# Performance work log

Hardware: AMD Instinct MI355X
Metric: run time of the kernel (lower is better)

Reference implementation:

```python
import jax, jax.numpy as jnp
import numpy as np

N_NODES = 100000
N_EDGES = 1200000
IN_DIM, HID_DIM, LAT_DIM = 128, 64, 32


def gcn_conv(x, W, b, src, dst, n_nodes):
    # PyG GCNConv with add_self_loops=True, symmetric normalization.
    # src/dst already include self loops.
    h = x @ W  # [N, out]
    deg = jax.ops.segment_sum(jnp.ones_like(dst, dtype=h.dtype), dst,
                              num_segments=n_nodes)  # includes self loop -> >=1
    dinv = jax.lax.rsqrt(deg)
    norm = dinv[src] * dinv[dst]  # [E]
    msg = h[src] * norm[:, None]  # gather + scale, [E, out]
    out = jax.ops.segment_sum(msg, dst, num_segments=n_nodes)  # scatter-add
    return out + b


def setup_inputs() -> dict:
    key = jax.random.key(0)
    ks = jax.random.split(key, 9)
    x = jax.random.normal(ks[0], (N_NODES, IN_DIM), dtype=jnp.float32)
    edge_index = jax.random.randint(ks[1], (2, N_EDGES), 0, N_NODES, dtype=jnp.int32)
    s1 = 1.0 / np.sqrt(IN_DIM)
    s2 = 1.0 / np.sqrt(HID_DIM)
    W1 = jax.random.uniform(ks[2], (IN_DIM, HID_DIM), jnp.float32, -s1, s1)
    b1 = jnp.zeros((HID_DIM,), jnp.float32)
    Wm = jax.random.uniform(ks[3], (HID_DIM, LAT_DIM), jnp.float32, -s2, s2)
    bm = jnp.zeros((LAT_DIM,), jnp.float32)
    Wv = jax.random.uniform(ks[4], (HID_DIM, LAT_DIM), jnp.float32, -s2, s2)
    bv = jnp.zeros((LAT_DIM,), jnp.float32)
    noise = jax.random.normal(ks[5], (N_NODES, LAT_DIM), dtype=jnp.float32)
    return {"x": x, "edge_index": edge_index, "W1": W1, "b1": b1,
            "Wm": Wm, "bm": bm, "Wv": Wv, "bv": bv, "noise": noise}


def reference(x, edge_index, W1, b1, Wm, bm, Wv, bv, noise):
    n = x.shape[0]
    loops = jnp.arange(n, dtype=edge_index.dtype)
    src = jnp.concatenate([edge_index[0], loops])
    dst = jnp.concatenate([edge_index[1], loops])
    h = jnp.tanh(gcn_conv(x, W1, b1, src, dst, n))
    mean = gcn_conv(h, Wm, bm, src, dst, n)
    logvar = gcn_conv(h, Wv, bv, src, dst, n)
    z = noise * jnp.exp(0.5 * logvar) + mean
    return (z, mean, logvar)
```

## Files before the change

kernel.cpp:

```cpp
#include <hip/hip_runtime.h>
#include <math.h>

#define TILE 4096
#define CSHIFT 10
#define CMASK 1023
#define NCMAX 128

typedef __attribute__((ext_vector_type(8))) short bf16x8;
typedef __attribute__((ext_vector_type(4))) float f32x4;
typedef __attribute__((ext_vector_type(2))) float f32x2;


__device__ __forceinline__ unsigned int pack_bf16(float a, float b) {
  unsigned int ua = __float_as_uint(a);
  ua += 0x7FFFu + ((ua >> 16) & 1u);
  unsigned int ub = __float_as_uint(b);
  ub += 0x7FFFu + ((ub >> 16) & 1u);
  return (ua >> 16) | (ub & 0xFFFF0000u);
}

__device__ __forceinline__ f32x2 shfl_xor2(f32x2 v, int m) {
  f32x2 r;
  r[0] = __shfl_xor(v[0], m);
  r[1] = __shfl_xor(v[1], m);
  return r;
}

__device__ __forceinline__ void add16_fp8_pk(f32x2* a2, uint4 hv) {
  unsigned int u[4] = {hv.x, hv.y, hv.z, hv.w};
#pragma unroll
  for (int i = 0; i < 4; ++i) {
    a2[2 * i]     += __builtin_amdgcn_cvt_pk_f32_fp8(u[i], false);
    a2[2 * i + 1] += __builtin_amdgcn_cvt_pk_f32_fp8(u[i], true);
  }
}

__device__ __forceinline__ void fma4(float4& acc, float s, const float4& w) {
  acc.x = fmaf(s, w.x, acc.x);
  acc.y = fmaf(s, w.y, acc.y);
  acc.z = fmaf(s, w.z, acc.z);
  acc.w = fmaf(s, w.w, acc.w);
}


__global__ __launch_bounds__(256) void coarse_hist_kernel(const int* __restrict__ dst,
    int* __restrict__ ccnt, int e) {
  __shared__ int h[NCMAX * 4];
  for (int i = threadIdx.x; i < NCMAX * 4; i += 256) h[i] = 0;
  __syncthreads();
  int rep = threadIdx.x & 3;
  for (int i = blockIdx.x * 256 + threadIdx.x; i < e; i += gridDim.x * 256)
    atomicAdd(&h[((dst[i] >> CSHIFT) << 2) | rep], 1);
  __syncthreads();
  for (int i = threadIdx.x; i < NCMAX; i += 256) {
    int s = h[i * 4] + h[i * 4 + 1] + h[i * 4 + 2] + h[i * 4 + 3];
    if (s) atomicAdd(&ccnt[i * 16], s);
  }
}

__global__ __launch_bounds__(64) void coarse_scan_kernel(const int* __restrict__ ccnt,
    int* __restrict__ coff, int* __restrict__ ccur, int* __restrict__ off,
    int nc, int n, int e) {
  int t = threadIdx.x;
  int ia = 2 * t, ib = 2 * t + 1;
  int va = ccnt[ia * 16];
  int vb = ccnt[ib * 16];
  int v = va + vb;
  int incl = v;
#pragma unroll
  for (int ofs = 1; ofs < 64; ofs <<= 1) {
    int w = __shfl_up(incl, ofs);
    if (t >= ofs) incl += w;
  }
  int ex = incl - v;
  coff[ia] = ex;      ccur[ia * 16] = ex;
  coff[ib] = ex + va; ccur[ib * 16] = ex + va;
  if (t == 63) coff[NCMAX] = incl;
  if (t == 0) off[n] = e;
}

__global__ __launch_bounds__(256) void coarse_partition_kernel(const int* __restrict__ src,
    const int* __restrict__ dst, int* __restrict__ ccur,
    unsigned int* __restrict__ packed, int e) {
  __shared__ unsigned int stage[TILE];
  __shared__ unsigned char bid[TILE];
  __shared__ int hist[NCMAX], excl[NCMAX], gbase[NCMAX], lcur[NCMAX];
  int ntiles = (e + TILE - 1) / TILE;
  for (int tile = blockIdx.x; tile < ntiles; tile += gridDim.x) {
    int i0 = tile * TILE;
    int cnt = e - i0; if (cnt > TILE) cnt = TILE;
    for (int i = threadIdx.x; i < NCMAX; i += 256) hist[i] = 0;
    __syncthreads();
    int myS[16], myD[16];
#pragma unroll
    for (int k = 0; k < 16; ++k) {
      int li = threadIdx.x + k * 256;
      if (li < cnt) {
        myS[k] = src[i0 + li];
        myD[k] = dst[i0 + li];
        atomicAdd(&hist[myD[k] >> CSHIFT], 1);
      }
    }
    __syncthreads();
    if (threadIdx.x < 64) {
      int t = threadIdx.x;
      int va = hist[2 * t], vb = hist[2 * t + 1];
      int v = va + vb;
      int incl = v;
#pragma unroll
      for (int ofs = 1; ofs < 64; ofs <<= 1) {
        int w = __shfl_up(incl, ofs);
        if (t >= ofs) incl += w;
      }
      int ex = incl - v;
      excl[2 * t] = ex;          lcur[2 * t] = ex;
      excl[2 * t + 1] = ex + va; lcur[2 * t + 1] = ex + va;
    }
    __syncthreads();
#pragma unroll
    for (int k = 0; k < 16; ++k) {
      int li = threadIdx.x + k * 256;
      if (li < cnt) {
        int c = myD[k] >> CSHIFT;
        int p = atomicAdd(&lcur[c], 1);
        stage[p] = (unsigned int)myS[k] | ((unsigned int)(myD[k] & CMASK) << 17);
        bid[p] = (unsigned char)c;
      }
    }
    __syncthreads();
    for (int i = threadIdx.x; i < NCMAX; i += 256) {
      int cc = lcur[i] - excl[i];
      gbase[i] = cc ? atomicAdd(&ccur[i * 16], cc) : 0;
    }
    __syncthreads();
    for (int i = threadIdx.x; i < cnt; i += 256) {
      int c = bid[i];
      packed[gbase[c] + (i - excl[c])] = stage[i];
    }
    __syncthreads();
  }
}

__global__ __launch_bounds__(512) void csr_fine_kernel(const unsigned int* __restrict__ packed,
    const int* __restrict__ coff, int* __restrict__ off, float* __restrict__ dinv,
    int* __restrict__ csr, int n) {
  __shared__ int lh[1024];
  __shared__ int lsum[512];
  int b = blockIdx.x;
  int t = threadIdx.x;
  int e0 = coff[b], e1 = coff[b + 1];
  int node0 = b << CSHIFT;
  for (int i = t; i < 1024; i += 512) lh[i] = 0;
  __syncthreads();
  for (int i = e0 + t; i < e1; i += 512) atomicAdd(&lh[packed[i] >> 17], 1);
  __syncthreads();
  int base = t * 2;
  int v0 = lh[base], v1 = lh[base + 1];
  int tsum = v0 + v1;
  lsum[t] = tsum;
  __syncthreads();
  for (int ofs = 1; ofs < 512; ofs <<= 1) {
    int add = (t >= ofs) ? lsum[t - ofs] : 0;
    __syncthreads();
    lsum[t] += add;
    __syncthreads();
  }
  int ex = lsum[t] - tsum;
  lh[base] = ex; lh[base + 1] = ex + v0;
  int node = node0 + base;
  if (node < n)     { off[node]     = e0 + ex;      dinv[node]     = rsqrtf((float)(v0 + 1)); }
  if (node + 1 < n) { off[node + 1] = e0 + ex + v0; dinv[node + 1] = rsqrtf((float)(v1 + 1)); }
  __syncthreads();
  for (int i = e0 + t; i < e1; i += 512) {
    unsigned int p = packed[i];
    int nl = p >> 17;
    int pos = atomicAdd(&lh[nl], 1);
    csr[e0 + pos] = (int)(p & 0x1FFFFu);
  }
}

__global__ __launch_bounds__(256) void gemm1_kernel(const float* __restrict__ x,
    const float* __restrict__ W1, const float* __restrict__ dinv,
    unsigned int* __restrict__ h1, int n) {
  __shared__ unsigned int xs[64 * 64];
  __shared__ unsigned int wt[64 * 64];
  for (int i = threadIdx.x; i < 4096; i += 256) {
    int c = i & 63, kp = i >> 6;
    float a = W1[(2 * kp) * 64 + c];
    float b = W1[(2 * kp + 1) * 64 + c];
    int slot = kp >> 2;
    int slotS = slot ^ (c & 7);
    wt[c * 64 + slotS * 4 + (kp & 3)] = pack_bf16(a, b);
  }
  int row0 = blockIdx.x * 64;
  int nrow = n - row0; if (nrow > 64) nrow = 64;
  for (int i = threadIdx.x; i < 64 * 32; i += 256) {
    int r = i >> 5, q = i & 31;
    float4 v = make_float4(0.f, 0.f, 0.f, 0.f);
    if (r < nrow) v = ((const float4*)(x + (size_t)(row0 + r) * 128))[q];
    int slot = q >> 1;
    int slotS = slot ^ (r & 7);
    int bi = r * 64 + slotS * 4 + (q & 1) * 2;
    xs[bi]     = pack_bf16(v.x, v.y);
    xs[bi + 1] = pack_bf16(v.z, v.w);
  }
  __syncthreads();
  int lane = threadIdx.x & 63;
  int w = threadIdx.x >> 6;
  int rl = lane & 15;
  int g = lane >> 4;
  f32x4 acc[4];
#pragma unroll
  for (int i = 0; i < 4; ++i) acc[i] = (f32x4){0.f, 0.f, 0.f, 0.f};
#pragma unroll
  for (int ks = 0; ks < 4; ++ks) {
    int as = ((ks * 4 + g) ^ (rl & 7)) * 4;
    bf16x8 af = *reinterpret_cast<const bf16x8*>(&xs[(w * 16 + rl) * 64 + as]);
#pragma unroll
    for (int nt = 0; nt < 4; ++nt) {
      int col = nt * 16 + rl;
      int bs = ((ks * 4 + g) ^ (col & 7)) * 4;
      bf16x8 bfr = *reinterpret_cast<const bf16x8*>(&wt[col * 64 + bs]);
      acc[nt] = __builtin_amdgcn_mfma_f32_16x16x32_bf16(af, bfr, acc[nt], 0, 0, 0);
    }
  }
#pragma unroll
  for (int i = 0; i < 4; ++i) {
    int row = row0 + w * 16 + g * 4 + i;
    float dv = (row < n) ? dinv[row] : 0.f;
#pragma unroll
    for (int nt = 0; nt < 4; ++nt) {
      float val = dv * acc[nt][i];
      float pv = __shfl_xor(val, 1);
      if (!(lane & 1) && row < n) {
        unsigned int pk = __builtin_amdgcn_cvt_pk_fp8_f32(val, pv, 0u, false);
        ((unsigned short*)h1)[(size_t)row * 32 + nt * 8 + (rl >> 1)] = (unsigned short)pk;
      }
    }
  }
}

template <int EPI>
__global__ __launch_bounds__(256) void agg_kernel(const uint4* __restrict__ h4,
    const int* __restrict__ off, const int* __restrict__ csr,
    const float* __restrict__ dinv, const float* __restrict__ bias,
    unsigned int* __restrict__ out, int n) {
  int lane = threadIdx.x & 63;
  int nd = lane >> 5;
  int j  = (lane >> 1) & 15;
  int fl = lane & 1;
  int node = blockIdx.x * 8 + (threadIdx.x >> 6) * 2 + nd;
  bool valid = node < n;
  f32x2 acc2[16];
#pragma unroll
  for (int i = 0; i < 16; ++i) acc2[i] = (f32x2){0.f, 0.f};
  if (valid) {
    if (j == 0) {
      const uint4* hp = &h4[(size_t)node * 4 + fl * 2];
      uint4 a = hp[0], b = hp[1];
      add16_fp8_pk(acc2, a); add16_fp8_pk(acc2 + 8, b);
    }
    int e1 = off[node + 1];
    for (int ee = off[node] + j; ee < e1; ee += 16) {
      int s = __builtin_nontemporal_load(&csr[ee]);
      const uint4* hp = &h4[(size_t)s * 4 + fl * 2];
      uint4 a = hp[0], b = hp[1];
      add16_fp8_pk(acc2, a); add16_fp8_pk(acc2 + 8, b);
    }
  }
#pragma unroll
  for (int i = 0; i < 8; ++i) {
    f32x2 tlo = acc2[i]     + shfl_xor2(acc2[i], 2);
    f32x2 thi = acc2[i + 8] + shfl_xor2(acc2[i + 8], 2);
    acc2[i] = (j & 1) ? thi : tlo;
  }
#pragma unroll
  for (int i = 0; i < 4; ++i) {
    f32x2 tlo = acc2[i]     + shfl_xor2(acc2[i], 4);
    f32x2 thi = acc2[i + 4] + shfl_xor2(acc2[i + 4], 4);
    acc2[i] = (j & 2) ? thi : tlo;
  }
#pragma unroll
  for (int i = 0; i < 2; ++i) {
    f32x2 tlo = acc2[i]     + shfl_xor2(acc2[i], 8);
    f32x2 thi = acc2[i + 2] + shfl_xor2(acc2[i + 2], 8);
    acc2[i] = (j & 4) ? thi : tlo;
  }
  {
    f32x2 tlo = acc2[0] + shfl_xor2(acc2[0], 16);
    f32x2 thi = acc2[1] + shfl_xor2(acc2[1], 16);
    acc2[0] = (j & 8) ? thi : tlo;
  }
  int q = 8 * (j & 1) + 4 * ((j >> 1) & 1) + 2 * ((j >> 2) & 1) + ((j >> 3) & 1);
  int f0 = fl * 32 + 2 * q;
  if (valid) {
    float di = dinv[node];
    if (EPI) {
      float v0 = di * tanhf(fmaf(di, acc2[0][0], bias[f0]));
      float v1 = di * tanhf(fmaf(di, acc2[0][1], bias[f0 + 1]));
      unsigned int pk = __builtin_amdgcn_cvt_pk_fp8_f32(v0, v1, 0u, false);
      ((unsigned short*)out)[(size_t)node * 32 + fl * 16 + q] = (unsigned short)pk;
    } else {
      float v0 = di * acc2[0][0];
      float v1 = di * acc2[0][1];
      out[(size_t)node * 32 + fl * 16 + q] = pack_bf16(v0, v1);
    }
  }
}

__global__ __launch_bounds__(256) void final_kernel(const unsigned int* __restrict__ aggb,
    const float* __restrict__ Wm, const float* __restrict__ bm,
    const float* __restrict__ Wv, const float* __restrict__ bv,
    const float* __restrict__ noise, float* __restrict__ outZ,
    float* __restrict__ outM, float* __restrict__ outLv, int n) {
  __shared__ float WmS[64 * 32];
  __shared__ float WvS[64 * 32];
  __shared__ float aggS[64 * 68];
  for (int i = threadIdx.x; i < 64 * 8; i += 256) {
    ((float4*)WmS)[i] = ((const float4*)Wm)[i];
    ((float4*)WvS)[i] = ((const float4*)Wv)[i];
  }
  int row0 = blockIdx.x * 64;
  int nrow = n - row0; if (nrow > 64) nrow = 64;
  for (int i = threadIdx.x; i < 64 * 16; i += 256) {
    int r = i >> 4, g = i & 15;
    uint2 u = make_uint2(0u, 0u);
    if (r < nrow) u = ((const uint2*)aggb)[(size_t)(row0 + r) * 16 + g];
    float* d = &aggS[r * 68 + g * 4];
    d[0] = __uint_as_float(u.x << 16);
    d[1] = __uint_as_float(u.x & 0xFFFF0000u);
    d[2] = __uint_as_float(u.y << 16);
    d[3] = __uint_as_float(u.y & 0xFFFF0000u);
  }
  __syncthreads();
  int c4 = (threadIdx.x & 7) * 4;
  int r2 = (threadIdx.x >> 3) * 2;
  float4 am[2], av[2];
#pragma unroll
  for (int i = 0; i < 2; ++i) {
    am[i] = make_float4(0.f, 0.f, 0.f, 0.f);
    av[i] = make_float4(0.f, 0.f, 0.f, 0.f);
  }
#pragma unroll 4
  for (int kq = 0; kq < 16; ++kq) {
    float4 xa[2], wm[4], wv[4];
#pragma unroll
    for (int i = 0; i < 2; ++i) xa[i] = *(const float4*)&aggS[(r2 + i) * 68 + kq * 4];
#pragma unroll
    for (int q = 0; q < 4; ++q) {
      wm[q] = *(const float4*)&WmS[(kq * 4 + q) * 32 + c4];
      wv[q] = *(const float4*)&WvS[(kq * 4 + q) * 32 + c4];
    }
#pragma unroll
    for (int i = 0; i < 2; ++i) {
      fma4(am[i], xa[i].x, wm[0]); fma4(am[i], xa[i].y, wm[1]);
      fma4(am[i], xa[i].z, wm[2]); fma4(am[i], xa[i].w, wm[3]);
      fma4(av[i], xa[i].x, wv[0]); fma4(av[i], xa[i].y, wv[1]);
      fma4(av[i], xa[i].z, wv[2]); fma4(av[i], xa[i].w, wv[3]);
    }
  }
  float4 bmv = *(const float4*)&bm[c4];
  float4 bvv = *(const float4*)&bv[c4];
#pragma unroll
  for (int i = 0; i < 2; ++i) {
    int row = row0 + r2 + i;
    if (row < n) {
      float4 m = am[i]; m.x += bmv.x; m.y += bmv.y; m.z += bmv.z; m.w += bmv.w;
      float4 v = av[i]; v.x += bvv.x; v.y += bvv.y; v.z += bvv.z; v.w += bvv.w;
      size_t oi = (size_t)row * 8 + (threadIdx.x & 7);
      float4 nz = ((const float4*)noise)[oi];
      float4 z;
      z.x = fmaf(nz.x, expf(0.5f * v.x), m.x);
      z.y = fmaf(nz.y, expf(0.5f * v.y), m.y);
      z.z = fmaf(nz.z, expf(0.5f * v.z), m.z);
      z.w = fmaf(nz.w, expf(0.5f * v.w), m.w);
      ((float4*)outZ)[oi] = z;
      ((float4*)outM)[oi] = m;
      ((float4*)outLv)[oi] = v;
    }
  }
}


extern "C" void kernel_launch(void* const* d_in, const int* in_sizes, int n_in,
                              void* d_out, int out_size, void* d_ws, size_t ws_size,
                              hipStream_t stream) {
  const float* x     = (const float*)d_in[0];
  const int*   edge  = (const int*)d_in[1];
  const float* W1    = (const float*)d_in[2];
  const float* b1    = (const float*)d_in[3];
  const float* Wm    = (const float*)d_in[4];
  const float* bm    = (const float*)d_in[5];
  const float* Wv    = (const float*)d_in[6];
  const float* bv    = (const float*)d_in[7];
  const float* noise = (const float*)d_in[8];
  int n = in_sizes[0] / 128;
  int e = in_sizes[1] / 2;
  const int* src = edge;
  const int* dst = edge + e;
  int nc = (n + CMASK) >> CSHIFT;

  int* ccnt = (int*)d_ws;
  int* ccur = ccnt + NCMAX * 16;
  int* coff = ccur + NCMAX * 16;
  int* off  = coff + (NCMAX + 4);
  float* dinv = (float*)(off + ((n + 4) & ~3));
  unsigned int* packed = (unsigned int*)(dinv + ((n + 3) & ~3));
  int* csr  = (int*)(packed + ((e + 3) & ~3));
  unsigned int* h1b = (unsigned int*)(csr + ((e + 3) & ~3));
  unsigned int* hb  = h1b + (size_t)n * 16;
  unsigned int* aggb = hb + (size_t)n * 16;

  float* outZ  = (float*)d_out;
  float* outM  = outZ + (size_t)n * 32;
  float* outLv = outM + (size_t)n * 32;

  int ntiles = (e + TILE - 1) / TILE;

  hipMemsetAsync(ccnt, 0, (size_t)NCMAX * 16 * sizeof(int), stream);
  coarse_hist_kernel<<<512, 256, 0, stream>>>(dst, ccnt, e);
  coarse_scan_kernel<<<1, 64, 0, stream>>>(ccnt, coff, ccur, off, nc, n, e);
  coarse_partition_kernel<<<ntiles, 256, 0, stream>>>(src, dst, ccur, packed, e);
  csr_fine_kernel<<<nc, 512, 0, stream>>>(packed, coff, off, dinv, csr, n);
  gemm1_kernel<<<(n + 63) / 64, 256, 0, stream>>>(x, W1, dinv, h1b, n);
  agg_kernel<1><<<(n + 7) / 8, 256, 0, stream>>>((const uint4*)h1b, off, csr, dinv, b1, hb, n);
  agg_kernel<0><<<(n + 7) / 8, 256, 0, stream>>>((const uint4*)hb, off, csr, dinv, b1, aggb, n);
  final_kernel<<<(n + 63) / 64, 256, 0, stream>>>(aggb, Wm, bm, Wv, bv, noise, outZ, outM, outLv, n);
}
```

Before: 170.4 us.

## Split hidden features into two half-width planes and aggregate each separately

The fp8 hidden features are stored as two separate 32-feature planes instead of one interleaved 64-feature row. Each aggregation layer now runs two passes, each gathering 32 bytes per neighbor instead of 64. The smaller per-pass working set is meant to fit better in L2/MALL and raise cache hit rates for random neighbor gathers. In exchange the CSR and offsets are read twice per layer and there are two extra kernel launches. The reduction tree is also shortened to match the 32-feature width.

```diff
diff --git a/kernel.cpp b/kernel.cpp
--- a/kernel.cpp
+++ b/kernel.cpp
@@ -181,7 +181,7 @@
 
 __global__ __launch_bounds__(256) void gemm1_kernel(const float* __restrict__ x,
     const float* __restrict__ W1, const float* __restrict__ dinv,
-    unsigned int* __restrict__ h1, int n) {
+    unsigned short* __restrict__ h1A, unsigned short* __restrict__ h1B, int n) {
   __shared__ unsigned int xs[64 * 64];
   __shared__ unsigned int wt[64 * 64];
   for (int i = threadIdx.x; i < 4096; i += 256) {
@@ -234,7 +234,8 @@
       float pv = __shfl_xor(val, 1);
       if (!(lane & 1) && row < n) {
         unsigned int pk = __builtin_amdgcn_cvt_pk_fp8_f32(val, pv, 0u, false);
-        ((unsigned short*)h1)[(size_t)row * 32 + nt * 8 + (rl >> 1)] = (unsigned short)pk;
+        unsigned short* dstp = (nt < 2) ? h1A : h1B;
+        dstp[(size_t)row * 16 + (nt & 1) * 8 + (rl >> 1)] = (unsigned short)pk;
       }
     }
   }
@@ -244,66 +245,59 @@
 __global__ __launch_bounds__(256) void agg_kernel(const uint4* __restrict__ h4,
     const int* __restrict__ off, const int* __restrict__ csr,
     const float* __restrict__ dinv, const float* __restrict__ bias,
-    unsigned int* __restrict__ out, int n) {
+    unsigned int* __restrict__ out, int n, int halfsel) {
   int lane = threadIdx.x & 63;
   int nd = lane >> 5;
   int j  = (lane >> 1) & 15;
   int fl = lane & 1;
   int node = blockIdx.x * 8 + (threadIdx.x >> 6) * 2 + nd;
   bool valid = node < n;
-  f32x2 acc2[16];
-#pragma unroll
-  for (int i = 0; i < 16; ++i) acc2[i] = (f32x2){0.f, 0.f};
+  f32x2 acc2[8];
+#pragma unroll
+  for (int i = 0; i < 8; ++i) acc2[i] = (f32x2){0.f, 0.f};
   if (valid) {
     if (j == 0) {
-      const uint4* hp = &h4[(size_t)node * 4 + fl * 2];
-      uint4 a = hp[0], b = hp[1];
-      add16_fp8_pk(acc2, a); add16_fp8_pk(acc2 + 8, b);
+      uint4 a = h4[(size_t)node * 2 + fl];
+      add16_fp8_pk(acc2, a);
     }
     int e1 = off[node + 1];
     for (int ee = off[node] + j; ee < e1; ee += 16) {
       int s = __builtin_nontemporal_load(&csr[ee]);
-      const uint4* hp = &h4[(size_t)s * 4 + fl * 2];
-      uint4 a = hp[0], b = hp[1];
-      add16_fp8_pk(acc2, a); add16_fp8_pk(acc2 + 8, b);
-    }
-  }
-#pragma unroll
-  for (int i = 0; i < 8; ++i) {
+      uint4 a = h4[(size_t)s * 2 + fl];
+      add16_fp8_pk(acc2, a);
+    }
+  }
+#pragma unroll
+  for (int i = 0; i < 4; ++i) {
     f32x2 tlo = acc2[i]     + shfl_xor2(acc2[i], 2);
-    f32x2 thi = acc2[i + 8] + shfl_xor2(acc2[i + 8], 2);
+    f32x2 thi = acc2[i + 4] + shfl_xor2(acc2[i + 4], 2);
     acc2[i] = (j & 1) ? thi : tlo;
   }
 #pragma unroll
-  for (int i = 0; i < 4; ++i) {
+  for (int i = 0; i < 2; ++i) {
     f32x2 tlo = acc2[i]     + shfl_xor2(acc2[i], 4);
-    f32x2 thi = acc2[i + 4] + shfl_xor2(acc2[i + 4], 4);
+    f32x2 thi = acc2[i + 2] + shfl_xor2(acc2[i + 2], 4);
     acc2[i] = (j & 2) ? thi : tlo;
   }
-#pragma unroll
-  for (int i = 0; i < 2; ++i) {
-    f32x2 tlo = acc2[i]     + shfl_xor2(acc2[i], 8);
-    f32x2 thi = acc2[i + 2] + shfl_xor2(acc2[i + 2], 8);
-    acc2[i] = (j & 4) ? thi : tlo;
-  }
   {
-    f32x2 tlo = acc2[0] + shfl_xor2(acc2[0], 16);
-    f32x2 thi = acc2[1] + shfl_xor2(acc2[1], 16);
-    acc2[0] = (j & 8) ? thi : tlo;
-  }
-  int q = 8 * (j & 1) + 4 * ((j >> 1) & 1) + 2 * ((j >> 2) & 1) + ((j >> 3) & 1);
-  int f0 = fl * 32 + 2 * q;
-  if (valid) {
+    f32x2 tlo = acc2[0] + shfl_xor2(acc2[0], 8);
+    f32x2 thi = acc2[1] + shfl_xor2(acc2[1], 8);
+    acc2[0] = (j & 4) ? thi : tlo;
+  }
+  acc2[0] = acc2[0] + shfl_xor2(acc2[0], 16);
+  int q3 = 4 * (j & 1) + 2 * ((j >> 1) & 1) + ((j >> 2) & 1);
+  int pidx = fl * 8 + q3;
+  if (valid && !(j & 8)) {
     float di = dinv[node];
     if (EPI) {
-      float v0 = di * tanhf(fmaf(di, acc2[0][0], bias[f0]));
-      float v1 = di * tanhf(fmaf(di, acc2[0][1], bias[f0 + 1]));
+      float v0 = di * tanhf(fmaf(di, acc2[0][0], bias[2 * pidx]));
+      float v1 = di * tanhf(fmaf(di, acc2[0][1], bias[2 * pidx + 1]));
       unsigned int pk = __builtin_amdgcn_cvt_pk_fp8_f32(v0, v1, 0u, false);
-      ((unsigned short*)out)[(size_t)node * 32 + fl * 16 + q] = (unsigned short)pk;
+      ((unsigned short*)out)[(size_t)node * 16 + pidx] = (unsigned short)pk;
     } else {
       float v0 = di * acc2[0][0];
       float v1 = di * acc2[0][1];
-      out[(size_t)node * 32 + fl * 16 + q] = pack_bf16(v0, v1);
+      out[(size_t)node * 32 + halfsel * 16 + pidx] = pack_bf16(v0, v1);
     }
   }
 }
@@ -407,23 +401,29 @@
   float* dinv = (float*)(off + ((n + 4) & ~3));
   unsigned int* packed = (unsigned int*)(dinv + ((n + 3) & ~3));
   int* csr  = (int*)(packed + ((e + 3) & ~3));
-  unsigned int* h1b = (unsigned int*)(csr + ((e + 3) & ~3));
-  unsigned int* hb  = h1b + (size_t)n * 16;
-  unsigned int* aggb = hb + (size_t)n * 16;
+  unsigned int* h1A = (unsigned int*)(csr + ((e + 3) & ~3));
+  unsigned int* h1B = h1A + (size_t)n * 8;
+  unsigned int* hbA = h1B + (size_t)n * 8;
+  unsigned int* hbB = hbA + (size_t)n * 8;
+  unsigned int* aggb = hbB + (size_t)n * 8;
 
   float* outZ  = (float*)d_out;
   float* outM  = outZ + (size_t)n * 32;
   float* outLv = outM + (size_t)n * 32;
 
   int ntiles = (e + TILE - 1) / TILE;
+  int aggGrid = (n + 7) / 8;
 
   hipMemsetAsync(ccnt, 0, (size_t)NCMAX * 16 * sizeof(int), stream);
   coarse_hist_kernel<<<512, 256, 0, stream>>>(dst, ccnt, e);
   coarse_scan_kernel<<<1, 64, 0, stream>>>(ccnt, coff, ccur, off, nc, n, e);
   coarse_partition_kernel<<<ntiles, 256, 0, stream>>>(src, dst, ccur, packed, e);
   csr_fine_kernel<<<nc, 512, 0, stream>>>(packed, coff, off, dinv, csr, n);
-  gemm1_kernel<<<(n + 63) / 64, 256, 0, stream>>>(x, W1, dinv, h1b, n);
-  agg_kernel<1><<<(n + 7) / 8, 256, 0, stream>>>((const uint4*)h1b, off, csr, dinv, b1, hb, n);
-  agg_kernel<0><<<(n + 7) / 8, 256, 0, stream>>>((const uint4*)hb, off, csr, dinv, b1, aggb, n);
+  gemm1_kernel<<<(n + 63) / 64, 256, 0, stream>>>(x, W1, dinv,
+      (unsigned short*)h1A, (unsigned short*)h1B, n);
+  agg_kernel<1><<<aggGrid, 256, 0, stream>>>((const uint4*)h1A, off, csr, dinv, b1,      hbA, n, 0);
+  agg_kernel<1><<<aggGrid, 256, 0, stream>>>((const uint4*)h1B, off, csr, dinv, b1 + 32, hbB, n, 1);
+  agg_kernel<0><<<aggGrid, 256, 0, stream>>>((const uint4*)hbA, off, csr, dinv, b1, aggb, n, 0);
+  agg_kernel<0><<<aggGrid, 256, 0, stream>>>((const uint4*)hbB, off, csr, dinv, b1, aggb, n, 1);
   final_kernel<<<(n + 63) / 64, 256, 0, stream>>>(aggb, Wm, bm, Wv, bv, noise, outZ, outM, outLv, n);
 }
```

Result: slower. 194.8 us (+14.3%).
